# Kernel tuning notes

Hardware: AMD Instinct MI355X
Metric: run time of the kernel (lower is better)

## Reference

```python
import jax, jax.numpy as jnp
import numpy as np

ALPHA = 0.2  # LeakyReLU negative slope

def setup_inputs() -> dict:
    key = jax.random.key(0)
    k_h, k_adj, k_W, k_a = jax.random.split(key, 4)
    B, N, F_in, F_out = 8, 2048, 256, 64
    h = jax.random.normal(k_h, (B, N, F_in), dtype=jnp.float32)
    adj = jax.random.randint(k_adj, (B, N, N), 0, 2, dtype=jnp.int32)
    # nn.Linear weights: W [F_out, F_in], a [1, 2*F_out]
    W = jax.random.normal(k_W, (F_out, F_in), dtype=jnp.float32) * (1.0 / np.sqrt(F_in))
    a = jax.random.normal(k_a, (1, 2 * F_out), dtype=jnp.float32) * (1.0 / np.sqrt(2 * F_out))
    return {"h": h, "adj": adj, "W": W, "a": a}

def reference(h, adj, W, a):
    # Wh = h @ W^T : [B, N, F_out]
    Wh = jnp.einsum('bnf,of->bno', h, W)
    F_out = Wh.shape[-1]
    # a([Wi, Wj]) decomposes: e_ij = a_i . Wh_i + a_j . Wh_j (no O(N^2 * 2F) concat)
    a_i = a[0, :F_out]   # [F_out]
    a_j = a[0, F_out:]   # [F_out]
    e_i = Wh @ a_i       # [B, N]
    e_j = Wh @ a_j       # [B, N]
    e = jax.nn.leaky_relu(e_i[:, :, None] + e_j[:, None, :], negative_slope=ALPHA)  # [B, N, N]
    e = jnp.where(adj == 0, -jnp.inf, e)
    att = jnp.nan_to_num(jax.nn.softmax(e, axis=-1), nan=0.0)
    # dropout is identity in eval mode
    return jnp.einsum('bnm,bmo->bno', att, Wh)
```

## Files before the change

kernel.cpp:

```cpp
#include <hip/hip_runtime.h>

typedef float f32x4 __attribute__((ext_vector_type(4)));
typedef __bf16 bf16x8 __attribute__((ext_vector_type(8)));
typedef unsigned short u16;
typedef unsigned int u32;

#define ALPHA 0.2f

__device__ __forceinline__ u16 f2bf(float x) {
    u32 u = __float_as_uint(x);
    u += 0x7FFFu + ((u >> 16) & 1u);
    return (u16)(u >> 16);
}

__global__ __launch_bounds__(256) void k_wh(
    const float* __restrict__ hsrc, const float* __restrict__ Wsrc,
    const float* __restrict__ asrc,
    u16* __restrict__ WhbT,
    float* __restrict__ ei, float* __restrict__ ej)
{
    __shared__ float Wl[64][68];
    __shared__ float hl[64][68];
    __shared__ __align__(16) u16 tl[4096];

    const int tid = threadIdx.x;
    const int tx = tid & 15, ty = tid >> 4;
    const int R0 = blockIdx.x * 64;

    float acc[4][4] = {};

    for (int kc = 0; kc < 4; ++kc) {
        const int k0 = kc * 64;
        __syncthreads();
        #pragma unroll
        for (int p = 0; p < 4; ++p) {
            int idx = p * 1024 + tid * 4;
            int row = idx >> 6, k = idx & 63;
            float4 wv4 = *reinterpret_cast<const float4*>(&Wsrc[row * 256 + k0 + k]);
            Wl[k + 0][row] = wv4.x; Wl[k + 1][row] = wv4.y;
            Wl[k + 2][row] = wv4.z; Wl[k + 3][row] = wv4.w;
            float4 hv4 = *reinterpret_cast<const float4*>(&hsrc[(size_t)(R0 + row) * 256 + k0 + k]);
            hl[k + 0][row] = hv4.x; hl[k + 1][row] = hv4.y;
            hl[k + 2][row] = hv4.z; hl[k + 3][row] = hv4.w;
        }
        __syncthreads();
        #pragma unroll 4
        for (int k = 0; k < 64; ++k) {
            float4 hv = *reinterpret_cast<const float4*>(&hl[k][4 * ty]);
            float4 wv = *reinterpret_cast<const float4*>(&Wl[k][4 * tx]);
            float hr[4] = {hv.x, hv.y, hv.z, hv.w};
            float wc[4] = {wv.x, wv.y, wv.z, wv.w};
            #pragma unroll
            for (int i = 0; i < 4; ++i)
                #pragma unroll
                for (int j = 0; j < 4; ++j)
                    acc[i][j] = fmaf(hr[i], wc[j], acc[i][j]);
        }
    }

    float4 av_i = *reinterpret_cast<const float4*>(&asrc[4 * tx]);
    float4 av_j = *reinterpret_cast<const float4*>(&asrc[64 + 4 * tx]);
    #pragma unroll
    for (int i = 0; i < 4; ++i) {
        float pi = acc[i][0]*av_i.x + acc[i][1]*av_i.y + acc[i][2]*av_i.z + acc[i][3]*av_i.w;
        float pj = acc[i][0]*av_j.x + acc[i][1]*av_j.y + acc[i][2]*av_j.z + acc[i][3]*av_j.w;
        #pragma unroll
        for (int off = 1; off < 16; off <<= 1) {
            pi += __shfl_xor(pi, off, 64);
            pj += __shfl_xor(pj, off, 64);
        }
        if (tx == 0) {
            ei[R0 + 4 * ty + i] = pi;
            ej[R0 + 4 * ty + i] = pj;
        }
    }

    #pragma unroll
    for (int i = 0; i < 4; ++i)
        #pragma unroll
        for (int j = 0; j < 4; ++j) {
            int row = 4 * tx + j;
            int col = 4 * ty + i;
            tl[(row * 64 + col) ^ ((row & 7) << 3)] = f2bf(acc[i][j]);
        }
    __syncthreads();
    {
        const int b = blockIdx.x >> 5;
        const int nloc = (blockIdx.x & 31) * 64;
        const int o = tid >> 2, rg = tid & 3;
        #pragma unroll
        for (int c = 0; c < 2; ++c) {
            int u = (o * 64 + rg * 16 + 8 * c) ^ ((o & 7) << 3);
            int4 v = *reinterpret_cast<const int4*>(&tl[u]);
            *reinterpret_cast<int4*>(&WhbT[(size_t)(b * 64 + o) * 2048 + nloc + rg * 16 + 8 * c]) = v;
        }
    }
}

__global__ __launch_bounds__(256) void k_mj(const float* __restrict__ ej, float* __restrict__ Mj)
{
    __shared__ float red[4];
    const int b = blockIdx.x, tid = threadIdx.x;
    float v = -1e30f;
    #pragma unroll
    for (int i = 0; i < 8; ++i) v = fmaxf(v, ej[b * 2048 + tid + 256 * i]);
    #pragma unroll
    for (int off = 1; off < 64; off <<= 1) v = fmaxf(v, __shfl_xor(v, off, 64));
    if ((tid & 63) == 0) red[tid >> 6] = v;
    __syncthreads();
    if (tid == 0) Mj[b] = fmaxf(fmaxf(red[0], red[1]), fmaxf(red[2], red[3]));
}

__global__ __launch_bounds__(256) void k_attn(
    const int* __restrict__ adj, const u16* __restrict__ WhbT,
    const float* __restrict__ ei_g, const float* __restrict__ ej_g,
    const float* __restrict__ Mj, float* __restrict__ out)
{
    __shared__ __align__(16) u16 p_lds[64 * 64];
    __shared__ __align__(16) u16 whT[80 * 64];
    __shared__ float Mrow[64];
    __shared__ float eis[64];

    const int tid  = threadIdx.x;
    const int lane = tid & 63;
    const int wid  = tid >> 6;
    const int b    = blockIdx.x >> 5;
    const int n0   = (blockIdx.x & 31) * 64;

    if (tid < 64) {
        float e = ei_g[b * 2048 + n0 + tid];
        eis[tid] = e;
        float x = e + Mj[b];
        Mrow[tid] = fmaxf(x, ALPHA * x);
    }
    #pragma unroll
    for (int i = 0; i < 4; ++i) {
        int row = 64 + wid + 4 * i;
        int m = lane;
        whT[(row * 64 + m) ^ ((row & 7) << 3)] = (row == 64) ? (u16)0x3F80 : (u16)0;
    }

    const int mA  = (tid & 15) * 4;
    const int rA  = tid >> 4;
    const int fW  = tid >> 2;
    const int mgW = tid & 3;

    const int* adjbase = adj + (size_t)(b * 2048 + n0) * 2048;
    const u16* wbase   = WhbT + (size_t)(b * 64) * 2048;

    int4 adjv[4]; float4 ejv; int4 wvv[2];
    auto LOADT = [&](int t) {
        const int m0 = t * 64;
        #pragma unroll
        for (int i = 0; i < 4; ++i)
            adjv[i] = *reinterpret_cast<const int4*>(&adjbase[(size_t)(rA + 16 * i) * 2048 + m0 + mA]);
        ejv = *reinterpret_cast<const float4*>(&ej_g[b * 2048 + m0 + mA]);
        #pragma unroll
        for (int c = 0; c < 2; ++c)
            wvv[c] = *reinterpret_cast<const int4*>(&wbase[(size_t)fW * 2048 + m0 + mgW * 16 + 8 * c]);
    };

    f32x4 acc[5] = {};
    LOADT(0);
    __syncthreads();

    for (int t = 0; t < 32; ++t) {
        #pragma unroll
        for (int i = 0; i < 4; ++i) {
            const int r = rA + 16 * i;
            const float eiv = eis[r];
            const float M = Mrow[r];
            const int am[4] = {adjv[i].x, adjv[i].y, adjv[i].z, adjv[i].w};
            const float ejs[4] = {ejv.x, ejv.y, ejv.z, ejv.w};
            u16 us[4];
            #pragma unroll
            for (int j = 0; j < 4; ++j) {
                float x = eiv + ejs[j];
                float lr = fmaxf(x, ALPHA * x);
                float p = __expf(lr - M);
                p = (am[j] != 0) ? p : 0.0f;
                us[j] = f2bf(p);
            }
            const int u = (r * 64 + mA) ^ ((r & 7) << 3);
            *reinterpret_cast<uint2*>(&p_lds[u]) =
                make_uint2((u32)us[0] | ((u32)us[1] << 16), (u32)us[2] | ((u32)us[3] << 16));
        }
        #pragma unroll
        for (int c = 0; c < 2; ++c) {
            const int u = (fW * 64 + mgW * 16 + 8 * c) ^ ((fW & 7) << 3);
            *reinterpret_cast<int4*>(&whT[u]) = wvv[c];
        }
        if (t < 31) LOADT(t + 1);
        __syncthreads();

        #pragma unroll
        for (int c = 0; c < 2; ++c) {
            const int row = 16 * wid + (lane & 15);
            const int kb = c * 32 + (lane >> 4) * 8;
            bf16x8 af = *reinterpret_cast<const bf16x8*>(&p_lds[(row * 64 + kb) ^ ((row & 7) << 3)]);
            #pragma unroll
            for (int fb = 0; fb < 5; ++fb) {
                const int f = fb * 16 + (lane & 15);
                bf16x8 bfr = *reinterpret_cast<const bf16x8*>(&whT[(f * 64 + kb) ^ ((f & 7) << 3)]);
                acc[fb] = __builtin_amdgcn_mfma_f32_16x16x32_bf16(af, bfr, acc[fb], 0, 0, 0);
            }
        }
        __syncthreads();
    }

    const int hi = lane >> 4, c0 = lane & 15;
    #pragma unroll
    for (int reg = 0; reg < 4; ++reg) {
        float sv = __shfl(acc[4][reg], lane & 48, 64);
        float inv = (sv > 0.0f) ? 1.0f / sv : 0.0f;
        const int n = n0 + 16 * wid + 4 * hi + reg;
        float* op = out + (size_t)(b * 2048 + n) * 64;
        #pragma unroll
        for (int fb = 0; fb < 4; ++fb)
            op[fb * 16 + c0] = acc[fb][reg] * inv;
    }
}

extern "C" void kernel_launch(void* const* d_in, const int* in_sizes, int n_in,
                              void* d_out, int out_size, void* d_ws, size_t ws_size,
                              hipStream_t stream)
{
    const float* h   = (const float*)d_in[0];
    const int*   adj = (const int*)d_in[1];
    const float* W   = (const float*)d_in[2];
    const float* a   = (const float*)d_in[3];
    float* out = (float*)d_out;

    u16*   WhbT = (u16*)d_ws;
    float* ei   = (float*)((char*)d_ws + 2 * 1024 * 1024);
    float* ej   = ei + 16384;
    float* Mj   = ej + 16384;

    k_wh<<<dim3(256), dim3(256), 0, stream>>>(h, W, a, WhbT, ei, ej);
    k_mj<<<dim3(8), dim3(256), 0, stream>>>(ej, Mj);
    k_attn<<<dim3(256), dim3(256), 0, stream>>>(adj, WhbT, ei, ej, Mj, out);
}
```

Measured before the change: 60.75 us.

## Halve attention row tile, fuse column-max into attention, use nontemporal adj loads

The attention kernel now handles 32 rows per block instead of 64, launching 512 blocks so more CUs are busy on the memory-bound adjacency stream. The four waves split the 5 MFMA feature blocks 3/2 across two row halves, and the denominator is passed between waves through shared memory. The separate k_mj launch is removed and each block recomputes the per-batch max of ej itself. Adjacency loads use nontemporal hints to avoid cache pollution. The cost is redundant Wh tile loads per block and an uneven MFMA split across waves.

New measurement: 75.94 us. +25.0%, slower.

```diff
diff --git a/kernel.cpp b/kernel.cpp
--- a/kernel.cpp
+++ b/kernel.cpp
@@ -2,6 +2,7 @@
 
 typedef float f32x4 __attribute__((ext_vector_type(4)));
 typedef __bf16 bf16x8 __attribute__((ext_vector_type(8)));
+typedef int i32x4 __attribute__((ext_vector_type(4)));
 typedef unsigned short u16;
 typedef unsigned int u32;
 
@@ -97,47 +98,47 @@
     }
 }
 
-__global__ __launch_bounds__(256) void k_mj(const float* __restrict__ ej, float* __restrict__ Mj)
-{
-    __shared__ float red[4];
-    const int b = blockIdx.x, tid = threadIdx.x;
-    float v = -1e30f;
-    #pragma unroll
-    for (int i = 0; i < 8; ++i) v = fmaxf(v, ej[b * 2048 + tid + 256 * i]);
-    #pragma unroll
-    for (int off = 1; off < 64; off <<= 1) v = fmaxf(v, __shfl_xor(v, off, 64));
-    if ((tid & 63) == 0) red[tid >> 6] = v;
-    __syncthreads();
-    if (tid == 0) Mj[b] = fmaxf(fmaxf(red[0], red[1]), fmaxf(red[2], red[3]));
-}
-
 __global__ __launch_bounds__(256) void k_attn(
     const int* __restrict__ adj, const u16* __restrict__ WhbT,
     const float* __restrict__ ei_g, const float* __restrict__ ej_g,
-    const float* __restrict__ Mj, float* __restrict__ out)
+    float* __restrict__ out)
 {
-    __shared__ __align__(16) u16 p_lds[64 * 64];
+    __shared__ __align__(16) u16 p_lds[32 * 64];
     __shared__ __align__(16) u16 whT[80 * 64];
-    __shared__ float Mrow[64];
-    __shared__ float eis[64];
+    __shared__ float Mrow[32];
+    __shared__ float eis[32];
+    __shared__ float sden[32];
+    __shared__ float red[4];
 
     const int tid  = threadIdx.x;
     const int lane = tid & 63;
     const int wid  = tid >> 6;
-    const int b    = blockIdx.x >> 5;
-    const int n0   = (blockIdx.x & 31) * 64;
-
-    if (tid < 64) {
+    const int b    = blockIdx.x >> 6;
+    const int n0   = (blockIdx.x & 63) * 32;
+
+    {
+        float4 v0 = *reinterpret_cast<const float4*>(&ej_g[b * 2048 + tid * 4]);
+        float4 v1 = *reinterpret_cast<const float4*>(&ej_g[b * 2048 + 1024 + tid * 4]);
+        float v = fmaxf(fmaxf(fmaxf(v0.x, v0.y), fmaxf(v0.z, v0.w)),
+                        fmaxf(fmaxf(v1.x, v1.y), fmaxf(v1.z, v1.w)));
+        #pragma unroll
+        for (int off = 1; off < 64; off <<= 1) v = fmaxf(v, __shfl_xor(v, off, 64));
+        if (lane == 0) red[wid] = v;
+    }
+    {
+        int row = 64 + (tid >> 4);
+        int m = (tid & 15) * 4;
+        u16 one = (row == 64) ? (u16)0x3F80 : (u16)0;
+        int u = (row * 64 + m) ^ ((row & 7) << 3);
+        whT[u + 0] = one; whT[u + 1] = one; whT[u + 2] = one; whT[u + 3] = one;
+    }
+    __syncthreads();
+    const float Mjv = fmaxf(fmaxf(red[0], red[1]), fmaxf(red[2], red[3]));
+    if (tid < 32) {
         float e = ei_g[b * 2048 + n0 + tid];
         eis[tid] = e;
-        float x = e + Mj[b];
+        float x = e + Mjv;
         Mrow[tid] = fmaxf(x, ALPHA * x);
-    }
-    #pragma unroll
-    for (int i = 0; i < 4; ++i) {
-        int row = 64 + wid + 4 * i;
-        int m = lane;
-        whT[(row * 64 + m) ^ ((row & 7) << 3)] = (row == 64) ? (u16)0x3F80 : (u16)0;
     }
 
     const int mA  = (tid & 15) * 4;
@@ -148,25 +149,31 @@
     const int* adjbase = adj + (size_t)(b * 2048 + n0) * 2048;
     const u16* wbase   = WhbT + (size_t)(b * 64) * 2048;
 
-    int4 adjv[4]; float4 ejv; int4 wvv[2];
+    i32x4 adjv[2]; float4 ejv; int4 wvv[2];
     auto LOADT = [&](int t) {
         const int m0 = t * 64;
         #pragma unroll
-        for (int i = 0; i < 4; ++i)
-            adjv[i] = *reinterpret_cast<const int4*>(&adjbase[(size_t)(rA + 16 * i) * 2048 + m0 + mA]);
+        for (int i = 0; i < 2; ++i)
+            adjv[i] = __builtin_nontemporal_load(
+                reinterpret_cast<const i32x4*>(&adjbase[(size_t)(rA + 16 * i) * 2048 + m0 + mA]));
         ejv = *reinterpret_cast<const float4*>(&ej_g[b * 2048 + m0 + mA]);
         #pragma unroll
         for (int c = 0; c < 2; ++c)
             wvv[c] = *reinterpret_cast<const int4*>(&wbase[(size_t)fW * 2048 + m0 + mgW * 16 + 8 * c]);
     };
 
-    f32x4 acc[5] = {};
+    const int rb  = wid & 1;
+    const int fbg = wid >> 1;
+    const int nfb = fbg ? 2 : 3;
+    const int fb0 = fbg ? 3 : 0;
+    f32x4 acc[3] = {};
+
     LOADT(0);
     __syncthreads();
 
     for (int t = 0; t < 32; ++t) {
         #pragma unroll
-        for (int i = 0; i < 4; ++i) {
+        for (int i = 0; i < 2; ++i) {
             const int r = rA + 16 * i;
             const float eiv = eis[r];
             const float M = Mrow[r];
@@ -195,29 +202,41 @@
 
         #pragma unroll
         for (int c = 0; c < 2; ++c) {
-            const int row = 16 * wid + (lane & 15);
+            const int row = 16 * rb + (lane & 15);
             const int kb = c * 32 + (lane >> 4) * 8;
             bf16x8 af = *reinterpret_cast<const bf16x8*>(&p_lds[(row * 64 + kb) ^ ((row & 7) << 3)]);
             #pragma unroll
-            for (int fb = 0; fb < 5; ++fb) {
-                const int f = fb * 16 + (lane & 15);
-                bf16x8 bfr = *reinterpret_cast<const bf16x8*>(&whT[(f * 64 + kb) ^ ((f & 7) << 3)]);
-                acc[fb] = __builtin_amdgcn_mfma_f32_16x16x32_bf16(af, bfr, acc[fb], 0, 0, 0);
+            for (int q = 0; q < 3; ++q) {
+                if (q < nfb) {
+                    const int f = (fb0 + q) * 16 + (lane & 15);
+                    bf16x8 bfr = *reinterpret_cast<const bf16x8*>(&whT[(f * 64 + kb) ^ ((f & 7) << 3)]);
+                    acc[q] = __builtin_amdgcn_mfma_f32_16x16x32_bf16(af, bfr, acc[q], 0, 0, 0);
+                }
             }
         }
         __syncthreads();
     }
 
     const int hi = lane >> 4, c0 = lane & 15;
+    if (fbg == 1 && c0 == 0) {
+        #pragma unroll
+        for (int reg = 0; reg < 4; ++reg)
+            sden[16 * rb + 4 * hi + reg] = acc[1][reg];
+    }
+    __syncthreads();
     #pragma unroll
     for (int reg = 0; reg < 4; ++reg) {
-        float sv = __shfl(acc[4][reg], lane & 48, 64);
+        const int r = 16 * rb + 4 * hi + reg;
+        float sv = sden[r];
         float inv = (sv > 0.0f) ? 1.0f / sv : 0.0f;
-        const int n = n0 + 16 * wid + 4 * hi + reg;
+        const int n = n0 + r;
         float* op = out + (size_t)(b * 2048 + n) * 64;
         #pragma unroll
-        for (int fb = 0; fb < 4; ++fb)
-            op[fb * 16 + c0] = acc[fb][reg] * inv;
+        for (int q = 0; q < 3; ++q) {
+            if (q < nfb && (fb0 + q) < 4) {
+                op[(fb0 + q) * 16 + c0] = acc[q][reg] * inv;
+            }
+        }
     }
 }
 
@@ -234,9 +253,7 @@
     u16*   WhbT = (u16*)d_ws;
     float* ei   = (float*)((char*)d_ws + 2 * 1024 * 1024);
     float* ej   = ei + 16384;
-    float* Mj   = ej + 16384;
 
     k_wh<<<dim3(256), dim3(256), 0, stream>>>(h, W, a, WhbT, ei, ej);
-    k_mj<<<dim3(8), dim3(256), 0, stream>>>(ej, Mj);
-    k_attn<<<dim3(256), dim3(256), 0, stream>>>(adj, WhbT, ei, ej, Mj, out);
-}
+    k_attn<<<dim3(512), dim3(256), 0, stream>>>(adj, WhbT, ei, ej, out);
+}
```

## Restructure attention kernel to register-direct MFMA operands with split-K waves

Applied to the files above, without the earlier changes.

Rewrites the attention kernel so each wave loads adj, ej and WhT fragments straight from global memory into MFMA operand registers, with no LDS staging and no per-tile barriers. It double-buffers the loads in registers, splits the key dimension across wave pairs, and reduces the two halves through LDS at the end. The column max of ej is now computed inside each wave, so the separate k_mj launch is gone. The grid doubles to 512 blocks of 32 rows. The cost is redundant per-wave global reads of WhT and ej and higher register pressure.

New measurement: 69.93 us. 1.15x slower.

```diff
diff --git a/kernel.cpp b/kernel.cpp
--- a/kernel.cpp
+++ b/kernel.cpp
@@ -2,6 +2,7 @@
 
 typedef float f32x4 __attribute__((ext_vector_type(4)));
 typedef __bf16 bf16x8 __attribute__((ext_vector_type(8)));
+typedef int i32x4 __attribute__((ext_vector_type(4)));
 typedef unsigned short u16;
 typedef unsigned int u32;
 
@@ -97,127 +98,131 @@
     }
 }
 
-__global__ __launch_bounds__(256) void k_mj(const float* __restrict__ ej, float* __restrict__ Mj)
-{
-    __shared__ float red[4];
-    const int b = blockIdx.x, tid = threadIdx.x;
-    float v = -1e30f;
-    #pragma unroll
-    for (int i = 0; i < 8; ++i) v = fmaxf(v, ej[b * 2048 + tid + 256 * i]);
-    #pragma unroll
-    for (int off = 1; off < 64; off <<= 1) v = fmaxf(v, __shfl_xor(v, off, 64));
-    if ((tid & 63) == 0) red[tid >> 6] = v;
-    __syncthreads();
-    if (tid == 0) Mj[b] = fmaxf(fmaxf(red[0], red[1]), fmaxf(red[2], red[3]));
-}
-
 __global__ __launch_bounds__(256) void k_attn(
     const int* __restrict__ adj, const u16* __restrict__ WhbT,
     const float* __restrict__ ei_g, const float* __restrict__ ej_g,
-    const float* __restrict__ Mj, float* __restrict__ out)
+    float* __restrict__ out)
 {
-    __shared__ __align__(16) u16 p_lds[64 * 64];
-    __shared__ __align__(16) u16 whT[80 * 64];
-    __shared__ float Mrow[64];
-    __shared__ float eis[64];
-
-    const int tid  = threadIdx.x;
-    const int lane = tid & 63;
-    const int wid  = tid >> 6;
-    const int b    = blockIdx.x >> 5;
-    const int n0   = (blockIdx.x & 31) * 64;
-
-    if (tid < 64) {
-        float e = ei_g[b * 2048 + n0 + tid];
-        eis[tid] = e;
-        float x = e + Mj[b];
-        Mrow[tid] = fmaxf(x, ALPHA * x);
-    }
-    #pragma unroll
-    for (int i = 0; i < 4; ++i) {
-        int row = 64 + wid + 4 * i;
-        int m = lane;
-        whT[(row * 64 + m) ^ ((row & 7) << 3)] = (row == 64) ? (u16)0x3F80 : (u16)0;
-    }
-
-    const int mA  = (tid & 15) * 4;
-    const int rA  = tid >> 4;
-    const int fW  = tid >> 2;
-    const int mgW = tid & 3;
-
-    const int* adjbase = adj + (size_t)(b * 2048 + n0) * 2048;
-    const u16* wbase   = WhbT + (size_t)(b * 64) * 2048;
-
-    int4 adjv[4]; float4 ejv; int4 wvv[2];
-    auto LOADT = [&](int t) {
-        const int m0 = t * 64;
-        #pragma unroll
-        for (int i = 0; i < 4; ++i)
-            adjv[i] = *reinterpret_cast<const int4*>(&adjbase[(size_t)(rA + 16 * i) * 2048 + m0 + mA]);
-        ejv = *reinterpret_cast<const float4*>(&ej_g[b * 2048 + m0 + mA]);
-        #pragma unroll
-        for (int c = 0; c < 2; ++c)
-            wvv[c] = *reinterpret_cast<const int4*>(&wbase[(size_t)fW * 2048 + m0 + mgW * 16 + 8 * c]);
-    };
-
-    f32x4 acc[5] = {};
-    LOADT(0);
+    __shared__ float accl[2][64][21];
+
+    const int tid   = threadIdx.x;
+    const int lane  = tid & 63;
+    const int wid   = tid >> 6;
+    const int b     = blockIdx.x >> 6;
+    const int blk   = blockIdx.x & 63;
+    const int strip = wid & 1;
+    const int half  = wid >> 1;
+    const int n0    = blk * 32 + strip * 16;
+    const int r     = lane & 15;
+    const int ks    = lane >> 4;
+
+    const int*   adjp = adj  + (size_t)(b * 2048 + n0 + r) * 2048 + half * 1024 + ks * 8;
+    const float* ejp  = ej_g + b * 2048 + half * 1024 + ks * 8;
+    const u16*   whp  = WhbT + (size_t)(b * 64 + r) * 2048 + half * 1024 + ks * 8;
+
+    i32x4 Aa0, Aa1, Ba0, Ba1;
+    float4 Ae0, Ae1, Be0, Be1;
+    bf16x8 Aw0, Aw1, Aw2, Aw3, Bw0, Bw1, Bw2, Bw3;
+
+#define LOADS(t, a0,a1,e0,e1,w0,w1,w2,w3) { \
+    const int mo_ = (t) * 32; \
+    a0 = *reinterpret_cast<const i32x4*>(adjp + mo_); \
+    a1 = *reinterpret_cast<const i32x4*>(adjp + mo_ + 4); \
+    e0 = *reinterpret_cast<const float4*>(ejp + mo_); \
+    e1 = *reinterpret_cast<const float4*>(ejp + mo_ + 4); \
+    w0 = *reinterpret_cast<const bf16x8*>(whp + mo_); \
+    w1 = *reinterpret_cast<const bf16x8*>(whp + 32768 + mo_); \
+    w2 = *reinterpret_cast<const bf16x8*>(whp + 65536 + mo_); \
+    w3 = *reinterpret_cast<const bf16x8*>(whp + 98304 + mo_); }
+
+    LOADS(0, Aa0,Aa1,Ae0,Ae1,Aw0,Aw1,Aw2,Aw3);
+    LOADS(1, Ba0,Ba1,Be0,Be1,Bw0,Bw1,Bw2,Bw3);
+
+    float mj = -1e30f;
+    #pragma unroll
+    for (int i = 0; i < 8; ++i) {
+        float4 v = *reinterpret_cast<const float4*>(&ej_g[b * 2048 + (i * 64 + lane) * 4]);
+        mj = fmaxf(mj, fmaxf(fmaxf(v.x, v.y), fmaxf(v.z, v.w)));
+    }
+    #pragma unroll
+    for (int off = 1; off < 64; off <<= 1) mj = fmaxf(mj, __shfl_xor(mj, off, 64));
+
+    const float eiv = ei_g[b * 2048 + n0 + r];
+    const float xM  = eiv + mj;
+    const float M   = fmaxf(xM, ALPHA * xM);
+
+    bf16x8 bones;
+    {
+        const float o = (r == 0) ? 1.0f : 0.0f;
+        #pragma unroll
+        for (int j = 0; j < 8; ++j) bones[j] = (__bf16)o;
+    }
+
+    f32x4 acc0 = {}, acc1 = {}, acc2 = {}, acc3 = {}, acc4 = {};
+
+#define PVAL(av, ev, dst) { \
+    float e_ = eiv + (ev); \
+    float lr_ = fmaxf(e_, ALPHA * e_); \
+    float p_ = __expf(lr_ - M); \
+    dst = (__bf16)(((av) != 0) ? p_ : 0.0f); }
+
+#define PSTEP(a0,a1,e0,e1,w0,w1,w2,w3) { \
+    bf16x8 af; \
+    PVAL(a0.x, e0.x, af[0]); PVAL(a0.y, e0.y, af[1]); \
+    PVAL(a0.z, e0.z, af[2]); PVAL(a0.w, e0.w, af[3]); \
+    PVAL(a1.x, e1.x, af[4]); PVAL(a1.y, e1.y, af[5]); \
+    PVAL(a1.z, e1.z, af[6]); PVAL(a1.w, e1.w, af[7]); \
+    acc0 = __builtin_amdgcn_mfma_f32_16x16x32_bf16(af, w0, acc0, 0, 0, 0); \
+    acc1 = __builtin_amdgcn_mfma_f32_16x16x32_bf16(af, w1, acc1, 0, 0, 0); \
+    acc2 = __builtin_amdgcn_mfma_f32_16x16x32_bf16(af, w2, acc2, 0, 0, 0); \
+    acc3 = __builtin_amdgcn_mfma_f32_16x16x32_bf16(af, w3, acc3, 0, 0, 0); \
+    acc4 = __builtin_amdgcn_mfma_f32_16x16x32_bf16(af, bones, acc4, 0, 0, 0); }
+
+    for (int k = 0; k < 15; ++k) {
+        const int t = 2 * k;
+        PSTEP(Aa0,Aa1,Ae0,Ae1,Aw0,Aw1,Aw2,Aw3);
+        LOADS(t + 2, Aa0,Aa1,Ae0,Ae1,Aw0,Aw1,Aw2,Aw3);
+        PSTEP(Ba0,Ba1,Be0,Be1,Bw0,Bw1,Bw2,Bw3);
+        LOADS(t + 3, Ba0,Ba1,Be0,Be1,Bw0,Bw1,Bw2,Bw3);
+    }
+    PSTEP(Aa0,Aa1,Ae0,Ae1,Aw0,Aw1,Aw2,Aw3);
+    PSTEP(Ba0,Ba1,Be0,Be1,Bw0,Bw1,Bw2,Bw3);
+
+#undef LOADS
+#undef PSTEP
+#undef PVAL
+
+    if (half == 1) {
+        #pragma unroll
+        for (int q = 0; q < 4; ++q) {
+            accl[strip][lane][q]      = acc0[q];
+            accl[strip][lane][4 + q]  = acc1[q];
+            accl[strip][lane][8 + q]  = acc2[q];
+            accl[strip][lane][12 + q] = acc3[q];
+            accl[strip][lane][16 + q] = acc4[q];
+        }
+    }
     __syncthreads();
-
-    for (int t = 0; t < 32; ++t) {
-        #pragma unroll
-        for (int i = 0; i < 4; ++i) {
-            const int r = rA + 16 * i;
-            const float eiv = eis[r];
-            const float M = Mrow[r];
-            const int am[4] = {adjv[i].x, adjv[i].y, adjv[i].z, adjv[i].w};
-            const float ejs[4] = {ejv.x, ejv.y, ejv.z, ejv.w};
-            u16 us[4];
-            #pragma unroll
-            for (int j = 0; j < 4; ++j) {
-                float x = eiv + ejs[j];
-                float lr = fmaxf(x, ALPHA * x);
-                float p = __expf(lr - M);
-                p = (am[j] != 0) ? p : 0.0f;
-                us[j] = f2bf(p);
-            }
-            const int u = (r * 64 + mA) ^ ((r & 7) << 3);
-            *reinterpret_cast<uint2*>(&p_lds[u]) =
-                make_uint2((u32)us[0] | ((u32)us[1] << 16), (u32)us[2] | ((u32)us[3] << 16));
-        }
-        #pragma unroll
-        for (int c = 0; c < 2; ++c) {
-            const int u = (fW * 64 + mgW * 16 + 8 * c) ^ ((fW & 7) << 3);
-            *reinterpret_cast<int4*>(&whT[u]) = wvv[c];
-        }
-        if (t < 31) LOADT(t + 1);
-        __syncthreads();
-
-        #pragma unroll
-        for (int c = 0; c < 2; ++c) {
-            const int row = 16 * wid + (lane & 15);
-            const int kb = c * 32 + (lane >> 4) * 8;
-            bf16x8 af = *reinterpret_cast<const bf16x8*>(&p_lds[(row * 64 + kb) ^ ((row & 7) << 3)]);
-            #pragma unroll
-            for (int fb = 0; fb < 5; ++fb) {
-                const int f = fb * 16 + (lane & 15);
-                bf16x8 bfr = *reinterpret_cast<const bf16x8*>(&whT[(f * 64 + kb) ^ ((f & 7) << 3)]);
-                acc[fb] = __builtin_amdgcn_mfma_f32_16x16x32_bf16(af, bfr, acc[fb], 0, 0, 0);
-            }
-        }
-        __syncthreads();
-    }
-
-    const int hi = lane >> 4, c0 = lane & 15;
-    #pragma unroll
-    for (int reg = 0; reg < 4; ++reg) {
-        float sv = __shfl(acc[4][reg], lane & 48, 64);
-        float inv = (sv > 0.0f) ? 1.0f / sv : 0.0f;
-        const int n = n0 + 16 * wid + 4 * hi + reg;
-        float* op = out + (size_t)(b * 2048 + n) * 64;
-        #pragma unroll
-        for (int fb = 0; fb < 4; ++fb)
-            op[fb * 16 + c0] = acc[fb][reg] * inv;
+    if (half == 0) {
+        #pragma unroll
+        for (int q = 0; q < 4; ++q) {
+            acc0[q] += accl[strip][lane][q];
+            acc1[q] += accl[strip][lane][4 + q];
+            acc2[q] += accl[strip][lane][8 + q];
+            acc3[q] += accl[strip][lane][12 + q];
+            acc4[q] += accl[strip][lane][16 + q];
+        }
+        #pragma unroll
+        for (int q = 0; q < 4; ++q) {
+            float d   = __shfl(acc4[q], lane & 48, 64);
+            float inv = (d > 0.0f) ? 1.0f / d : 0.0f;
+            const int n = n0 + ks * 4 + q;
+            float* op = out + (size_t)(b * 2048 + n) * 64 + r;
+            op[0]  = acc0[q] * inv;
+            op[16] = acc1[q] * inv;
+            op[32] = acc2[q] * inv;
+            op[48] = acc3[q] * inv;
+        }
     }
 }
 
@@ -234,9 +239,7 @@
     u16*   WhbT = (u16*)d_ws;
     float* ei   = (float*)((char*)d_ws + 2 * 1024 * 1024);
     float* ej   = ei + 16384;
-    float* Mj   = ej + 16384;
 
     k_wh<<<dim3(256), dim3(256), 0, stream>>>(h, W, a, WhbT, ei, ej);
-    k_mj<<<dim3(8), dim3(256), 0, stream>>>(ej, Mj);
-    k_attn<<<dim3(256), dim3(256), 0, stream>>>(adj, WhbT, ei, ej, Mj, out);
-}
+    k_attn<<<dim3(512), dim3(256), 0, stream>>>(adj, WhbT, ei, ej, out);
+}
```
